# Optimization experiments

Measured on AMD Instinct MI355X. Metric: run time of the kernel, lower is better.

## Reference

```python
import jax, jax.numpy as jnp
import numpy as np

B, L, D, H = 2, 2048, 1024, 16
HD = D // H  # head_dim = 64


def _clin(xr, xi, Wr, br, Wi, bi):
    # (x_r + i x_i)(W_r + i W_i): out_r = fc_r(x_r) - fc_i(x_i); out_i = fc_r(x_i) + fc_i(x_r)
    rr = xr @ Wr.T + br
    ii = xi @ Wi.T + bi
    ri = xi @ Wr.T + br
    ir = xr @ Wi.T + bi
    return rr - ii, ri + ir


def _heads(x):
    # [B, L, D] -> [B, H, L, HD]
    return x.reshape(B, L, H, HD).transpose(0, 2, 1, 3)


def setup_inputs() -> dict:
    key = jax.random.key(0)
    ks = jax.random.split(key, 11)
    inp = {
        "x_r": jax.random.normal(ks[0], (B, L, D), jnp.float32),
        "x_i": jax.random.normal(ks[1], (B, L, D), jnp.float32),
        "attention_mask": jnp.zeros((B, 1, 1, L), jnp.float32),
    }
    names = ["Wq_r", "Wq_i", "Wk_r", "Wk_i", "Wv_r", "Wv_i", "Wo_r", "Wo_i"]
    for n, k in zip(names, ks[2:10]):
        inp[n] = jax.random.normal(k, (D, D), jnp.float32) * 0.02
        inp["b" + n[1:]] = jnp.zeros((D,), jnp.float32)
    return inp


def reference(x_r, x_i, attention_mask,
              Wq_r, bq_r, Wq_i, bq_i,
              Wk_r, bk_r, Wk_i, bk_i,
              Wv_r, bv_r, Wv_i, bv_i,
              Wo_r, bo_r, Wo_i, bo_i):
    qr, qi = _clin(x_r, x_i, Wq_r, bq_r, Wq_i, bq_i)
    kr, ki = _clin(x_r, x_i, Wk_r, bk_r, Wk_i, bk_i)
    vr, vi = _clin(x_r, x_i, Wv_r, bv_r, Wv_i, bv_i)
    q_r, q_i = _heads(qr), _heads(qi)
    k_r, k_i = _heads(kr), _heads(ki)
    v_r, v_i = _heads(vr), _heads(vi)
    # complex QK^T cross terms -> squared-magnitude interference score
    s_real = jnp.einsum('bhqd,bhkd->bhqk', q_r, k_r) + jnp.einsum('bhqd,bhkd->bhqk', q_i, k_i)
    s_imag = jnp.einsum('bhqd,bhkd->bhqk', q_i, k_r) - jnp.einsum('bhqd,bhkd->bhqk', q_r, k_i)
    interference = (s_real * s_real + s_imag * s_imag) / HD + attention_mask
    attn = jax.nn.softmax(interference, axis=-1)
    c_r = jnp.einsum('bhqk,bhkd->bhqd', attn, v_r).transpose(0, 2, 1, 3).reshape(B, L, D)
    c_i = jnp.einsum('bhqk,bhkd->bhqd', attn, v_i).transpose(0, 2, 1, 3).reshape(B, L, D)
    out_r, out_i = _clin(c_r, c_i, Wo_r, bo_r, Wo_i, bo_i)
    return out_r, out_i
```

## Files before the change

kernel.cpp:

```cpp
#include <hip/hip_runtime.h>
#include <hip/hip_bf16.h>

typedef unsigned short u16;
typedef __attribute__((ext_vector_type(8))) short bf16x8;
typedef __attribute__((ext_vector_type(8))) _Float16 f16x8;
typedef __attribute__((ext_vector_type(8))) unsigned short u16x8;
typedef __attribute__((ext_vector_type(4))) float f32x4;

__device__ __forceinline__ u16 f2b(float f) {
  _Float16 h = (_Float16)f;
  return __builtin_bit_cast(u16, h);
}

__device__ __forceinline__ f32x4 mfma16(bf16x8 a, bf16x8 b, f32x4 c) {
  return __builtin_amdgcn_mfma_f32_16x16x32_f16(
      __builtin_bit_cast(f16x8, a), __builtin_bit_cast(f16x8, b), c, 0, 0, 0);
}

#define GLD16(dst, src) __builtin_amdgcn_global_load_lds( \
    (const __attribute__((address_space(1))) void*)(src), \
    (__attribute__((address_space(3))) void*)(dst), 16, 0, 0)

__global__ void pack_x_kernel(u16* __restrict__ A1, const float* __restrict__ xr,
                              const float* __restrict__ xi) {
  const int id = blockIdx.x * 256 + threadIdx.x;
  const size_t k8 = (size_t)id * 8;
  const int n = (int)(k8 >> 11);
  const int kk = (int)(k8 & 2047);
  const float* src = (kk < 1024) ? (xr + (size_t)n * 1024 + kk)
                                 : (xi + (size_t)n * 1024 + (kk - 1024));
  float4 a = *(const float4*)src;
  float4 c = *(const float4*)(src + 4);
  u16x8 o;
  o[0] = f2b(a.x); o[1] = f2b(a.y); o[2] = f2b(a.z); o[3] = f2b(a.w);
  o[4] = f2b(c.x); o[5] = f2b(c.y); o[6] = f2b(c.z); o[7] = f2b(c.w);
  *(u16x8*)(A1 + k8) = o;
}

__global__ void pack_w_kernel(u16* __restrict__ dst, float* __restrict__ biasDst,
                              const float* __restrict__ Wr, const float* __restrict__ Wi,
                              const float* __restrict__ br, const float* __restrict__ bi,
                              int isim) {
  const int row = blockIdx.x;
  const int kk = threadIdx.x * 8;
  const int half = kk >> 10;
  const int kloc = kk & 1023;
  const float* W = (half == 0) ? (isim ? Wi : Wr) : (isim ? Wr : Wi);
  const float sgn = (half == 1 && !isim) ? -1.f : 1.f;
  const float* src = W + (size_t)row * 1024 + kloc;
  float4 a = *(const float4*)src;
  float4 c = *(const float4*)(src + 4);
  u16x8 o;
  o[0] = f2b(sgn * a.x); o[1] = f2b(sgn * a.y); o[2] = f2b(sgn * a.z); o[3] = f2b(sgn * a.w);
  o[4] = f2b(sgn * c.x); o[5] = f2b(sgn * c.y); o[6] = f2b(sgn * c.z); o[7] = f2b(sgn * c.w);
  *(u16x8*)(dst + (size_t)row * 2048 + kk) = o;
  if (threadIdx.x == 0)
    biasDst[row] = isim ? (br[row] + bi[row]) : (br[row] - bi[row]);
}

template<int OUT_F32>
__global__ __launch_bounds__(256) void gemm_bt(const u16* __restrict__ A,
                                               const u16* __restrict__ Bw,
                                               const float* __restrict__ bias,
                                               void* __restrict__ outp) {
  constexpr int K = 2048;
  __shared__ __align__(16) u16 As[128 * 64];
  __shared__ __align__(16) u16 Bs[128 * 64];
  const int tid = threadIdx.x;
  const int w = tid >> 6, l = tid & 63;
  const int l15 = l & 15, lhi = l >> 4;
  const int m0 = blockIdx.y * 128, n0 = blockIdx.x * 128;
  const int wm = w >> 1, wn = w & 1;
  f32x4 acc[4][4] = {};
  for (int kt = 0; kt < K; kt += 64) {
#pragma unroll
    for (int it = 0; it < 4; ++it) {
      const int grp = it * 4 + w;
      const int cl = grp * 64 + l;
      const int r = cl >> 3;
      const int g = (cl & 7) ^ (r & 7);
      GLD16(As + grp * 512, A + (size_t)(m0 + r) * K + kt + g * 8);
      GLD16(Bs + grp * 512, Bw + (size_t)(n0 + r) * K + kt + g * 8);
    }
    __syncthreads();
#pragma unroll
    for (int ks = 0; ks < 2; ++ks) {
      const int c = ks * 4 + lhi;
      bf16x8 af[4], bfr[4];
#pragma unroll
      for (int mf = 0; mf < 4; ++mf) {
        const int r = wm * 64 + mf * 16 + l15;
        af[mf] = *(const bf16x8*)&As[r * 64 + ((c ^ (r & 7)) << 3)];
      }
#pragma unroll
      for (int nf = 0; nf < 4; ++nf) {
        const int r = wn * 64 + nf * 16 + l15;
        bfr[nf] = *(const bf16x8*)&Bs[r * 64 + ((c ^ (r & 7)) << 3)];
      }
#pragma unroll
      for (int mf = 0; mf < 4; ++mf)
#pragma unroll
        for (int nf = 0; nf < 4; ++nf)
          acc[mf][nf] = mfma16(af[mf], bfr[nf], acc[mf][nf]);
    }
    __syncthreads();
  }
#pragma unroll
  for (int nf = 0; nf < 4; ++nf) {
    const int j = n0 + wn * 64 + nf * 16 + l15;
    const float bv = bias[j];
    const size_t obase = (size_t)(j >> 10) * (4096 * 1024) + (j & 1023);
#pragma unroll
    for (int mf = 0; mf < 4; ++mf) {
#pragma unroll
      for (int i = 0; i < 4; ++i) {
        const int row = m0 + wm * 64 + mf * 16 + lhi * 4 + i;
        const float v = acc[mf][nf][i] + bv;
        if constexpr (OUT_F32) ((float*)outp)[obase + (size_t)row * 1024] = v;
        else                   ((u16*)outp)[obase + (size_t)row * 1024] = f2b(v);
      }
    }
  }
}

__global__ void transpose_v_kernel(const u16* __restrict__ v, u16* __restrict__ vt) {
  __shared__ u16 tile[64 * 65];
  const int tt = blockIdx.x, bh = blockIdx.y, ri = blockIdx.z;
  const int b = bh >> 4, h = bh & 15;
  const size_t M1 = (size_t)4096 * 1024;
  const u16* src = v + (size_t)ri * M1;
  u16* dst = vt + (size_t)ri * 32 * 64 * 2048;
  const int t0 = tt * 64;
#pragma unroll
  for (int e = 0; e < 16; ++e) {
    const int id = e * 256 + threadIdx.x;
    const int row = id >> 6, col = id & 63;
    tile[row * 65 + col] = src[(size_t)(b * 2048 + t0 + row) * 1024 + h * 64 + col];
  }
  __syncthreads();
#pragma unroll
  for (int e = 0; e < 16; ++e) {
    const int id = e * 256 + threadIdx.x;
    const int d = id >> 6, tok = id & 63;
    dst[((size_t)bh * 64 + d) * 2048 + t0 + tok] = tile[tok * 65 + d];
  }
}

__global__ __launch_bounds__(256) void attn_kernel(const u16* __restrict__ qkv,
                                                   const u16* __restrict__ vt,
                                                   const float* __restrict__ mask,
                                                   u16* __restrict__ A2) {
  __shared__ __align__(16) u16 KVb[2][4][64 * 64];
  __shared__ __align__(16) u16 Pl[4 * 16 * 72];
  const int tid = threadIdx.x, w = tid >> 6, l = tid & 63;
  const int l15 = l & 15, lhi = l >> 4;
  const int q0 = blockIdx.x * 64;
  const int bh = blockIdx.y;
  const int b = bh >> 4, h = bh & 15;
  const size_t M1 = (size_t)4096 * 1024;
  const u16* qr_b = qkv;
  const u16* qi_b = qkv + M1;
  const u16* kr_b = qkv + 2 * M1;
  const u16* ki_b = qkv + 3 * M1;
  const u16* vtr = vt;
  const u16* vti = vt + (size_t)32 * 64 * 2048;

  const size_t qrow = (size_t)(b * 2048 + q0 + w * 16 + l15) * 1024 + h * 64;
  bf16x8 qr[2], qi[2], qrn[2];
#pragma unroll
  for (int ks = 0; ks < 2; ++ks) {
    qr[ks] = *(const bf16x8*)&qr_b[qrow + ks * 32 + lhi * 8];
    qi[ks] = *(const bf16x8*)&qi_b[qrow + ks * 32 + lhi * 8];
    qrn[ks] = qr[ks] ^ (short)0x8000;
  }
  float mrow[4], srow[4];
  f32x4 o_r[4] = {}, o_i[4] = {};
#pragma unroll
  for (int i = 0; i < 4; ++i) { mrow[i] = -1e30f; srow[i] = 0.f; }
  u16* Pw = Pl + w * (16 * 72);

  auto STAGE = [&](int tile, int bufi) {
    const int k0s = tile * 64;
#pragma unroll
    for (int it = 0; it < 2; ++it) {
      const int grp = it * 4 + w;
      const int cl = grp * 64 + l;
      const int r = cl >> 3;
      const int g = (cl & 7) ^ (r & 7);
      const size_t krow = (size_t)(b * 2048 + k0s + r) * 1024 + h * 64 + g * 8;
      const size_t vrow = (size_t)(bh * 64 + r) * 2048 + k0s + g * 8;
      GLD16(&KVb[bufi][0][grp * 512], kr_b + krow);
      GLD16(&KVb[bufi][1][grp * 512], ki_b + krow);
      GLD16(&KVb[bufi][2][grp * 512], vtr + vrow);
      GLD16(&KVb[bufi][3][grp * 512], vti + vrow);
    }
  };

  STAGE(0, 0);
  for (int kt = 0; kt < 32; ++kt) {
    const int cur = kt & 1;
    const int k0 = kt * 64;
    __syncthreads();
    if (kt < 31) STAGE(kt + 1, cur ^ 1);
    const u16* Kr = &KVb[cur][0][0];
    const u16* Ki = &KVb[cur][1][0];
    const u16* Vr = &KVb[cur][2][0];
    const u16* Vi = &KVb[cur][3][0];
    f32x4 sr[4] = {}, si[4] = {};
    __builtin_amdgcn_s_setprio(1);
#pragma unroll
    for (int nf = 0; nf < 4; ++nf) {
      const int krr = nf * 16 + l15;
      const int sw = krr & 7;
#pragma unroll
      for (int ks = 0; ks < 2; ++ks) {
        const int c = ks * 4 + lhi;
        const int off = krr * 64 + ((c ^ sw) << 3);
        bf16x8 kfr = *(const bf16x8*)&Kr[off];
        bf16x8 kfi = *(const bf16x8*)&Ki[off];
        sr[nf] = mfma16(qr[ks], kfr, sr[nf]);
        sr[nf] = mfma16(qi[ks], kfi, sr[nf]);
        si[nf] = mfma16(qi[ks], kfr, si[nf]);
        si[nf] = mfma16(qrn[ks], kfi, si[nf]);
      }
    }
    __builtin_amdgcn_s_setprio(0);
    float t[4][4];
#pragma unroll
    for (int nf = 0; nf < 4; ++nf) {
      const float mk = mask[b * 2048 + k0 + nf * 16 + l15];
#pragma unroll
      for (int i = 0; i < 4; ++i)
        t[nf][i] = (sr[nf][i] * sr[nf][i] + si[nf][i] * si[nf][i]) * 0.015625f + mk;
    }
    float pmax[4];
#pragma unroll
    for (int i = 0; i < 4; ++i) {
      float v = fmaxf(fmaxf(t[0][i], t[1][i]), fmaxf(t[2][i], t[3][i]));
      v = fmaxf(v, __shfl_xor(v, 1, 64));
      v = fmaxf(v, __shfl_xor(v, 2, 64));
      v = fmaxf(v, __shfl_xor(v, 4, 64));
      v = fmaxf(v, __shfl_xor(v, 8, 64));
      pmax[i] = v;
    }
    bool grow = false;
#pragma unroll
    for (int i = 0; i < 4; ++i) grow |= (pmax[i] > mrow[i] + 8.f);
    if (__any(grow)) {
#pragma unroll
      for (int i = 0; i < 4; ++i) {
        const float mn = fmaxf(mrow[i], pmax[i]);
        const float sc = __expf(mrow[i] - mn);
        mrow[i] = mn;
        srow[i] *= sc;
#pragma unroll
        for (int nf = 0; nf < 4; ++nf) { o_r[nf][i] *= sc; o_i[nf][i] *= sc; }
      }
    }
    float p[4][4];
#pragma unroll
    for (int nf = 0; nf < 4; ++nf)
#pragma unroll
      for (int i = 0; i < 4; ++i) {
        p[nf][i] = __expf(t[nf][i] - mrow[i]);
        srow[i] += p[nf][i];
      }
#pragma unroll
    for (int nf = 0; nf < 4; ++nf)
#pragma unroll
      for (int i = 0; i < 4; ++i)
        Pw[(lhi * 4 + i) * 72 + nf * 16 + l15] = f2b(p[nf][i]);
    __builtin_amdgcn_s_setprio(1);
#pragma unroll
    for (int ks = 0; ks < 2; ++ks) {
      bf16x8 pa = *(const bf16x8*)&Pw[l15 * 72 + ks * 32 + lhi * 8];
      const int c = ks * 4 + lhi;
#pragma unroll
      for (int nf = 0; nf < 4; ++nf) {
        const int vr = nf * 16 + l15;
        const int off = vr * 64 + ((c ^ (vr & 7)) << 3);
        bf16x8 vfr = *(const bf16x8*)&Vr[off];
        bf16x8 vfi = *(const bf16x8*)&Vi[off];
        o_r[nf] = mfma16(pa, vfr, o_r[nf]);
        o_i[nf] = mfma16(pa, vfi, o_i[nf]);
      }
    }
    __builtin_amdgcn_s_setprio(0);
  }
  float inv[4];
#pragma unroll
  for (int i = 0; i < 4; ++i) {
    float v = srow[i];
    v += __shfl_xor(v, 1, 64);
    v += __shfl_xor(v, 2, 64);
    v += __shfl_xor(v, 4, 64);
    v += __shfl_xor(v, 8, 64);
    inv[i] = 1.f / v;
  }
  const int rowbase = b * 2048 + q0 + w * 16 + lhi * 4;
#pragma unroll
  for (int nf = 0; nf < 4; ++nf) {
    const int col = h * 64 + nf * 16 + l15;
#pragma unroll
    for (int i = 0; i < 4; ++i) {
      const size_t rw = (size_t)(rowbase + i) * 2048;
      A2[rw + col] = f2b(o_r[nf][i] * inv[i]);
      A2[rw + 1024 + col] = f2b(o_i[nf][i] * inv[i]);
    }
  }
}

extern "C" void kernel_launch(void* const* d_in, const int* in_sizes, int n_in,
                              void* d_out, int out_size, void* d_ws, size_t ws_size,
                              hipStream_t stream) {
  (void)in_sizes; (void)n_in; (void)out_size; (void)ws_size;
  const float* x_r  = (const float*)d_in[0];
  const float* x_i  = (const float*)d_in[1];
  const float* mask = (const float*)d_in[2];
  const float* Wq_r = (const float*)d_in[3];
  const float* bq_r = (const float*)d_in[4];
  const float* Wq_i = (const float*)d_in[5];
  const float* bq_i = (const float*)d_in[6];
  const float* Wk_r = (const float*)d_in[7];
  const float* bk_r = (const float*)d_in[8];
  const float* Wk_i = (const float*)d_in[9];
  const float* bk_i = (const float*)d_in[10];
  const float* Wv_r = (const float*)d_in[11];
  const float* bv_r = (const float*)d_in[12];
  const float* Wv_i = (const float*)d_in[13];
  const float* bv_i = (const float*)d_in[14];
  const float* Wo_r = (const float*)d_in[15];
  const float* bo_r = (const float*)d_in[16];
  const float* Wo_i = (const float*)d_in[17];
  const float* bo_i = (const float*)d_in[18];

  char* ws = (char*)d_ws;
  const size_t M1 = (size_t)4096 * 1024;
  u16* A    = (u16*)(ws);
  u16* B1   = (u16*)(ws + (16u << 20));
  u16* vt   = (u16*)(ws + (16u << 20));
  u16* B2   = (u16*)(ws + (32u << 20));
  u16* qkv  = (u16*)(ws + (40u << 20));
  float* bias1 = (float*)(ws + (88u << 20));
  float* bias2 = (float*)(ws + (88u << 20) + (1u << 15));

  pack_x_kernel<<<4096, 256, 0, stream>>>(A, x_r, x_i);
  pack_w_kernel<<<1024, 256, 0, stream>>>(B1 + 0 * (size_t)1024 * 2048, bias1 + 0,    Wq_r, Wq_i, bq_r, bq_i, 0);
  pack_w_kernel<<<1024, 256, 0, stream>>>(B1 + 1 * (size_t)1024 * 2048, bias1 + 1024, Wq_r, Wq_i, bq_r, bq_i, 1);
  pack_w_kernel<<<1024, 256, 0, stream>>>(B1 + 2 * (size_t)1024 * 2048, bias1 + 2048, Wk_r, Wk_i, bk_r, bk_i, 0);
  pack_w_kernel<<<1024, 256, 0, stream>>>(B1 + 3 * (size_t)1024 * 2048, bias1 + 3072, Wk_r, Wk_i, bk_r, bk_i, 1);
  pack_w_kernel<<<1024, 256, 0, stream>>>(B1 + 4 * (size_t)1024 * 2048, bias1 + 4096, Wv_r, Wv_i, bv_r, bv_i, 0);
  pack_w_kernel<<<1024, 256, 0, stream>>>(B1 + 5 * (size_t)1024 * 2048, bias1 + 5120, Wv_r, Wv_i, bv_r, bv_i, 1);

  gemm_bt<0><<<dim3(48, 32), 256, 0, stream>>>(A, B1, bias1, qkv);

  transpose_v_kernel<<<dim3(32, 32, 2), 256, 0, stream>>>(qkv + 4 * M1, vt);
  pack_w_kernel<<<1024, 256, 0, stream>>>(B2,                      bias2,        Wo_r, Wo_i, bo_r, bo_i, 0);
  pack_w_kernel<<<1024, 256, 0, stream>>>(B2 + (size_t)1024 * 2048, bias2 + 1024, Wo_r, Wo_i, bo_r, bo_i, 1);

  attn_kernel<<<dim3(32, 32), 256, 0, stream>>>(qkv, vt, mask, A);

  gemm_bt<1><<<dim3(16, 32), 256, 0, stream>>>(A, B2, bias2, d_out);
}
```

Measured before the change: 478.2 us.

## Fuse V transpose into QKV GEMM epilogue, batch weight packing, shrink attention tiles

The QKV GEMM epilogue now writes V directly in transposed layout, which removes the separate transpose kernel. Weight packing is batched into two grid launches instead of eight. The attention kernel drops to 32-key tiles with a per-wave staging split, a smaller LDS footprint and launch bounds targeting 4 blocks per CU. Softmax now runs in base 2 via v_exp_f32 with the log2e scale folded into the score constant, and the rescale threshold is raised to match. Smaller tiles mean twice as many iterations and barriers, which may offset the occupancy gain.

After: 486.5 us. Within noise of the previous version (+1.7%).

```diff
diff --git a/kernel.cpp b/kernel.cpp
--- a/kernel.cpp
+++ b/kernel.cpp
@@ -15,6 +15,10 @@
 __device__ __forceinline__ f32x4 mfma16(bf16x8 a, bf16x8 b, f32x4 c) {
   return __builtin_amdgcn_mfma_f32_16x16x32_f16(
       __builtin_bit_cast(f16x8, a), __builtin_bit_cast(f16x8, b), c, 0, 0, 0);
+}
+
+__device__ __forceinline__ float fexp2(float x) {
+  float r; asm("v_exp_f32 %0, %1" : "=v"(r) : "v"(x)); return r;
 }
 
 #define GLD16(dst, src) __builtin_amdgcn_global_load_lds( \
@@ -37,32 +41,44 @@
   *(u16x8*)(A1 + k8) = o;
 }
 
-__global__ void pack_w_kernel(u16* __restrict__ dst, float* __restrict__ biasDst,
-                              const float* __restrict__ Wr, const float* __restrict__ Wi,
-                              const float* __restrict__ br, const float* __restrict__ bi,
-                              int isim) {
+struct PWArgs {
+  const float* Wr[4]; const float* Wi[4];
+  const float* br[4]; const float* bi[4];
+};
+
+__global__ void pack_w_all(PWArgs a, int sbase, u16* __restrict__ B1,
+                           u16* __restrict__ B2, float* __restrict__ bias1,
+                           float* __restrict__ bias2) {
+  const int s = sbase + blockIdx.y;
+  const int wi = s >> 1, isim = s & 1;
+  u16* dst = (s < 6) ? (B1 + (size_t)s * (1024 * 2048))
+                     : (B2 + (size_t)(s - 6) * (1024 * 2048));
+  float* biasDst = (s < 6) ? (bias1 + s * 1024) : (bias2 + (s - 6) * 1024);
   const int row = blockIdx.x;
   const int kk = threadIdx.x * 8;
   const int half = kk >> 10;
   const int kloc = kk & 1023;
-  const float* W = (half == 0) ? (isim ? Wi : Wr) : (isim ? Wr : Wi);
+  const float* W = (half == 0) ? (isim ? a.Wi[wi] : a.Wr[wi])
+                               : (isim ? a.Wr[wi] : a.Wi[wi]);
   const float sgn = (half == 1 && !isim) ? -1.f : 1.f;
   const float* src = W + (size_t)row * 1024 + kloc;
-  float4 a = *(const float4*)src;
+  float4 x = *(const float4*)src;
   float4 c = *(const float4*)(src + 4);
   u16x8 o;
-  o[0] = f2b(sgn * a.x); o[1] = f2b(sgn * a.y); o[2] = f2b(sgn * a.z); o[3] = f2b(sgn * a.w);
+  o[0] = f2b(sgn * x.x); o[1] = f2b(sgn * x.y); o[2] = f2b(sgn * x.z); o[3] = f2b(sgn * x.w);
   o[4] = f2b(sgn * c.x); o[5] = f2b(sgn * c.y); o[6] = f2b(sgn * c.z); o[7] = f2b(sgn * c.w);
   *(u16x8*)(dst + (size_t)row * 2048 + kk) = o;
   if (threadIdx.x == 0)
-    biasDst[row] = isim ? (br[row] + bi[row]) : (br[row] - bi[row]);
-}
-
-template<int OUT_F32>
+    biasDst[row] = isim ? (a.br[wi][row] + a.bi[wi][row])
+                        : (a.br[wi][row] - a.bi[wi][row]);
+}
+
+template<int MODE>
 __global__ __launch_bounds__(256) void gemm_bt(const u16* __restrict__ A,
                                                const u16* __restrict__ Bw,
                                                const float* __restrict__ bias,
-                                               void* __restrict__ outp) {
+                                               void* __restrict__ outp,
+                                               u16* __restrict__ vtp) {
   constexpr int K = 2048;
   __shared__ __align__(16) u16 As[128 * 64];
   __shared__ __align__(16) u16 Bs[128 * 64];
@@ -109,49 +125,49 @@
   for (int nf = 0; nf < 4; ++nf) {
     const int j = n0 + wn * 64 + nf * 16 + l15;
     const float bv = bias[j];
-    const size_t obase = (size_t)(j >> 10) * (4096 * 1024) + (j & 1023);
-#pragma unroll
-    for (int mf = 0; mf < 4; ++mf) {
-#pragma unroll
-      for (int i = 0; i < 4; ++i) {
-        const int row = m0 + wm * 64 + mf * 16 + lhi * 4 + i;
-        const float v = acc[mf][nf][i] + bv;
-        if constexpr (OUT_F32) ((float*)outp)[obase + (size_t)row * 1024] = v;
-        else                   ((u16*)outp)[obase + (size_t)row * 1024] = f2b(v);
-      }
-    }
-  }
-}
-
-__global__ void transpose_v_kernel(const u16* __restrict__ v, u16* __restrict__ vt) {
-  __shared__ u16 tile[64 * 65];
-  const int tt = blockIdx.x, bh = blockIdx.y, ri = blockIdx.z;
-  const int b = bh >> 4, h = bh & 15;
-  const size_t M1 = (size_t)4096 * 1024;
-  const u16* src = v + (size_t)ri * M1;
-  u16* dst = vt + (size_t)ri * 32 * 64 * 2048;
-  const int t0 = tt * 64;
-#pragma unroll
-  for (int e = 0; e < 16; ++e) {
-    const int id = e * 256 + threadIdx.x;
-    const int row = id >> 6, col = id & 63;
-    tile[row * 65 + col] = src[(size_t)(b * 2048 + t0 + row) * 1024 + h * 64 + col];
-  }
-  __syncthreads();
-#pragma unroll
-  for (int e = 0; e < 16; ++e) {
-    const int id = e * 256 + threadIdx.x;
-    const int d = id >> 6, tok = id & 63;
-    dst[((size_t)bh * 64 + d) * 2048 + t0 + tok] = tile[tok * 65 + d];
-  }
-}
-
-__global__ __launch_bounds__(256) void attn_kernel(const u16* __restrict__ qkv,
-                                                   const u16* __restrict__ vt,
-                                                   const float* __restrict__ mask,
-                                                   u16* __restrict__ A2) {
-  __shared__ __align__(16) u16 KVb[2][4][64 * 64];
-  __shared__ __align__(16) u16 Pl[4 * 16 * 72];
+    if constexpr (MODE == 1) {
+      const size_t obase = (size_t)(j >> 10) * (4096 * 1024) + (j & 1023);
+#pragma unroll
+      for (int mf = 0; mf < 4; ++mf)
+#pragma unroll
+        for (int i = 0; i < 4; ++i) {
+          const int row = m0 + wm * 64 + mf * 16 + lhi * 4 + i;
+          ((float*)outp)[obase + (size_t)row * 1024] = acc[mf][nf][i] + bv;
+        }
+    } else {
+      if (j < 4096) {
+        const size_t obase = (size_t)(j >> 10) * (4096 * 1024) + (j & 1023);
+#pragma unroll
+        for (int mf = 0; mf < 4; ++mf)
+#pragma unroll
+          for (int i = 0; i < 4; ++i) {
+            const int row = m0 + wm * 64 + mf * 16 + lhi * 4 + i;
+            ((u16*)outp)[obase + (size_t)row * 1024] = f2b(acc[mf][nf][i] + bv);
+          }
+      } else {
+        const int jv = j - 4096;
+        const size_t vb = (size_t)(jv >> 10) * 4194304 +
+                          (size_t)((jv >> 6) & 15) * 131072 +
+                          (size_t)(jv & 63) * 2048;
+#pragma unroll
+        for (int mf = 0; mf < 4; ++mf)
+#pragma unroll
+          for (int i = 0; i < 4; ++i) {
+            const int row = m0 + wm * 64 + mf * 16 + lhi * 4 + i;
+            const int b2 = row >> 11, tok = row & 2047;
+            vtp[vb + (size_t)b2 * 2097152 + tok] = f2b(acc[mf][nf][i] + bv);
+          }
+      }
+    }
+  }
+}
+
+__global__ __launch_bounds__(256, 4) void attn_kernel(const u16* __restrict__ qkv,
+                                                      const u16* __restrict__ vt,
+                                                      const float* __restrict__ mask,
+                                                      u16* __restrict__ A2) {
+  __shared__ __align__(16) u16 KVb[2][4][2048];
+  __shared__ __align__(16) u16 Pl[4][16 * 40];
   const int tid = threadIdx.x, w = tid >> 6, l = tid & 63;
   const int l15 = l & 15, lhi = l >> 4;
   const int q0 = blockIdx.x * 64;
@@ -164,6 +180,8 @@
   const u16* ki_b = qkv + 3 * M1;
   const u16* vtr = vt;
   const u16* vti = vt + (size_t)32 * 64 * 2048;
+  constexpr float LOG2E = 1.4426950408889634f;
+  constexpr float C2 = 0.015625f * LOG2E;
 
   const size_t qrow = (size_t)(b * 2048 + q0 + w * 16 + l15) * 1024 + h * 64;
   bf16x8 qr[2], qi[2], qrn[2];
@@ -177,45 +195,54 @@
   f32x4 o_r[4] = {}, o_i[4] = {};
 #pragma unroll
   for (int i = 0; i < 4; ++i) { mrow[i] = -1e30f; srow[i] = 0.f; }
-  u16* Pw = Pl + w * (16 * 72);
+  u16* Pw = Pl[w];
 
   auto STAGE = [&](int tile, int bufi) {
-    const int k0s = tile * 64;
-#pragma unroll
-    for (int it = 0; it < 2; ++it) {
-      const int grp = it * 4 + w;
-      const int cl = grp * 64 + l;
-      const int r = cl >> 3;
-      const int g = (cl & 7) ^ (r & 7);
-      const size_t krow = (size_t)(b * 2048 + k0s + r) * 1024 + h * 64 + g * 8;
-      const size_t vrow = (size_t)(bh * 64 + r) * 2048 + k0s + g * 8;
-      GLD16(&KVb[bufi][0][grp * 512], kr_b + krow);
-      GLD16(&KVb[bufi][1][grp * 512], ki_b + krow);
-      GLD16(&KVb[bufi][2][grp * 512], vtr + vrow);
-      GLD16(&KVb[bufi][3][grp * 512], vti + vrow);
+    const int k0s = tile * 32;
+    if (w < 2) {
+      const u16* src = w ? ki_b : kr_b;
+      u16* dstb = &KVb[bufi][w][0];
+#pragma unroll
+      for (int it = 0; it < 4; ++it) {
+        const int cl = it * 64 + l;
+        const int r = cl >> 3;
+        const int g = (cl & 7) ^ (r & 7);
+        GLD16(dstb + it * 512, src + (size_t)(b * 2048 + k0s + r) * 1024 + h * 64 + g * 8);
+      }
+    } else {
+      const u16* src = (w == 3) ? vti : vtr;
+      u16* dstb = &KVb[bufi][w][0];
+#pragma unroll
+      for (int it = 0; it < 4; ++it) {
+        const int cl = it * 64 + l;
+        const int r = cl >> 2;
+        const int g = (cl & 3) ^ ((r >> 1) & 3);
+        GLD16(dstb + it * 512, src + (size_t)(bh * 64 + r) * 2048 + k0s + g * 8);
+      }
     }
   };
 
   STAGE(0, 0);
-  for (int kt = 0; kt < 32; ++kt) {
+#pragma unroll 2
+  for (int kt = 0; kt < 64; ++kt) {
     const int cur = kt & 1;
-    const int k0 = kt * 64;
+    const int k0 = kt * 32;
     __syncthreads();
-    if (kt < 31) STAGE(kt + 1, cur ^ 1);
+    if (kt < 63) STAGE(kt + 1, cur ^ 1);
     const u16* Kr = &KVb[cur][0][0];
     const u16* Ki = &KVb[cur][1][0];
     const u16* Vr = &KVb[cur][2][0];
     const u16* Vi = &KVb[cur][3][0];
-    f32x4 sr[4] = {}, si[4] = {};
+    f32x4 sr[2] = {}, si[2] = {};
     __builtin_amdgcn_s_setprio(1);
 #pragma unroll
-    for (int nf = 0; nf < 4; ++nf) {
-      const int krr = nf * 16 + l15;
-      const int sw = krr & 7;
+    for (int nf = 0; nf < 2; ++nf) {
+      const int rk = nf * 16 + l15;
+      const int sw = rk & 7;
 #pragma unroll
       for (int ks = 0; ks < 2; ++ks) {
         const int c = ks * 4 + lhi;
-        const int off = krr * 64 + ((c ^ sw) << 3);
+        const int off = rk * 64 + ((c ^ sw) << 3);
         bf16x8 kfr = *(const bf16x8*)&Kr[off];
         bf16x8 kfi = *(const bf16x8*)&Ki[off];
         sr[nf] = mfma16(qr[ks], kfr, sr[nf]);
@@ -225,18 +252,20 @@
       }
     }
     __builtin_amdgcn_s_setprio(0);
-    float t[4][4];
-#pragma unroll
-    for (int nf = 0; nf < 4; ++nf) {
-      const float mk = mask[b * 2048 + k0 + nf * 16 + l15];
-#pragma unroll
-      for (int i = 0; i < 4; ++i)
-        t[nf][i] = (sr[nf][i] * sr[nf][i] + si[nf][i] * si[nf][i]) * 0.015625f + mk;
+    float t[2][4];
+#pragma unroll
+    for (int nf = 0; nf < 2; ++nf) {
+      const float mkl = mask[b * 2048 + k0 + nf * 16 + l15] * LOG2E;
+#pragma unroll
+      for (int i = 0; i < 4; ++i) {
+        const float ss = fmaf(si[nf][i], si[nf][i], sr[nf][i] * sr[nf][i]);
+        t[nf][i] = fmaf(ss, C2, mkl);
+      }
     }
     float pmax[4];
 #pragma unroll
     for (int i = 0; i < 4; ++i) {
-      float v = fmaxf(fmaxf(t[0][i], t[1][i]), fmaxf(t[2][i], t[3][i]));
+      float v = fmaxf(t[0][i], t[1][i]);
       v = fmaxf(v, __shfl_xor(v, 1, 64));
       v = fmaxf(v, __shfl_xor(v, 2, 64));
       v = fmaxf(v, __shfl_xor(v, 4, 64));
@@ -245,45 +274,41 @@
     }
     bool grow = false;
 #pragma unroll
-    for (int i = 0; i < 4; ++i) grow |= (pmax[i] > mrow[i] + 8.f);
+    for (int i = 0; i < 4; ++i) grow |= (pmax[i] > mrow[i] + 11.f);
     if (__any(grow)) {
 #pragma unroll
       for (int i = 0; i < 4; ++i) {
         const float mn = fmaxf(mrow[i], pmax[i]);
-        const float sc = __expf(mrow[i] - mn);
+        const float sc = fexp2(mrow[i] - mn);
         mrow[i] = mn;
         srow[i] *= sc;
 #pragma unroll
         for (int nf = 0; nf < 4; ++nf) { o_r[nf][i] *= sc; o_i[nf][i] *= sc; }
       }
     }
-    float p[4][4];
-#pragma unroll
-    for (int nf = 0; nf < 4; ++nf)
+    float p[2][4];
+#pragma unroll
+    for (int nf = 0; nf < 2; ++nf)
 #pragma unroll
       for (int i = 0; i < 4; ++i) {
-        p[nf][i] = __expf(t[nf][i] - mrow[i]);
+        p[nf][i] = fexp2(t[nf][i] - mrow[i]);
         srow[i] += p[nf][i];
       }
 #pragma unroll
-    for (int nf = 0; nf < 4; ++nf)
+    for (int nf = 0; nf < 2; ++nf)
 #pragma unroll
       for (int i = 0; i < 4; ++i)
-        Pw[(lhi * 4 + i) * 72 + nf * 16 + l15] = f2b(p[nf][i]);
+        Pw[(lhi * 4 + i) * 40 + nf * 16 + l15] = f2b(p[nf][i]);
+    bf16x8 pa = *(const bf16x8*)&Pw[l15 * 40 + lhi * 8];
     __builtin_amdgcn_s_setprio(1);
 #pragma unroll
-    for (int ks = 0; ks < 2; ++ks) {
-      bf16x8 pa = *(const bf16x8*)&Pw[l15 * 72 + ks * 32 + lhi * 8];
-      const int c = ks * 4 + lhi;
-#pragma unroll
-      for (int nf = 0; nf < 4; ++nf) {
-        const int vr = nf * 16 + l15;
-        const int off = vr * 64 + ((c ^ (vr & 7)) << 3);
-        bf16x8 vfr = *(const bf16x8*)&Vr[off];
-        bf16x8 vfi = *(const bf16x8*)&Vi[off];
-        o_r[nf] = mfma16(pa, vfr, o_r[nf]);
-        o_i[nf] = mfma16(pa, vfi, o_i[nf]);
-      }
+    for (int nf = 0; nf < 4; ++nf) {
+      const int d = nf * 16 + l15;
+      const int off = d * 32 + ((lhi ^ ((d >> 1) & 3)) << 3);
+      bf16x8 vfr = *(const bf16x8*)&Vr[off];
+      bf16x8 vfi = *(const bf16x8*)&Vi[off];
+      o_r[nf] = mfma16(pa, vfr, o_r[nf]);
+      o_i[nf] = mfma16(pa, vfi, o_i[nf]);
     }
     __builtin_amdgcn_s_setprio(0);
   }
@@ -317,48 +342,34 @@
   const float* x_r  = (const float*)d_in[0];
   const float* x_i  = (const float*)d_in[1];
   const float* mask = (const float*)d_in[2];
-  const float* Wq_r = (const float*)d_in[3];
-  const float* bq_r = (const float*)d_in[4];
-  const float* Wq_i = (const float*)d_in[5];
-  const float* bq_i = (const float*)d_in[6];
-  const float* Wk_r = (const float*)d_in[7];
-  const float* bk_r = (const float*)d_in[8];
-  const float* Wk_i = (const float*)d_in[9];
-  const float* bk_i = (const float*)d_in[10];
-  const float* Wv_r = (const float*)d_in[11];
-  const float* bv_r = (const float*)d_in[12];
-  const float* Wv_i = (const float*)d_in[13];
-  const float* bv_i = (const float*)d_in[14];
-  const float* Wo_r = (const float*)d_in[15];
-  const float* bo_r = (const float*)d_in[16];
-  const float* Wo_i = (const float*)d_in[17];
-  const float* bo_i = (const float*)d_in[18];
+
+  PWArgs pw;
+  pw.Wr[0] = (const float*)d_in[3];  pw.br[0] = (const float*)d_in[4];
+  pw.Wi[0] = (const float*)d_in[5];  pw.bi[0] = (const float*)d_in[6];
+  pw.Wr[1] = (const float*)d_in[7];  pw.br[1] = (const float*)d_in[8];
+  pw.Wi[1] = (const float*)d_in[9];  pw.bi[1] = (const float*)d_in[10];
+  pw.Wr[2] = (const float*)d_in[11]; pw.br[2] = (const float*)d_in[12];
+  pw.Wi[2] = (const float*)d_in[13]; pw.bi[2] = (const float*)d_in[14];
+  pw.Wr[3] = (const float*)d_in[15]; pw.br[3] = (const float*)d_in[16];
+  pw.Wi[3] = (const float*)d_in[17]; pw.bi[3] = (const float*)d_in[18];
 
   char* ws = (char*)d_ws;
-  const size_t M1 = (size_t)4096 * 1024;
-  u16* A    = (u16*)(ws);
-  u16* B1   = (u16*)(ws + (16u << 20));
-  u16* vt   = (u16*)(ws + (16u << 20));
-  u16* B2   = (u16*)(ws + (32u << 20));
-  u16* qkv  = (u16*)(ws + (40u << 20));
+  u16* A     = (u16*)(ws);
+  u16* B1    = (u16*)(ws + (16u << 20));
+  u16* B2    = (u16*)(ws + (16u << 20));
+  u16* qkvp  = (u16*)(ws + (40u << 20));
+  u16* vtp   = (u16*)(ws + (72u << 20));
   float* bias1 = (float*)(ws + (88u << 20));
   float* bias2 = (float*)(ws + (88u << 20) + (1u << 15));
 
   pack_x_kernel<<<4096, 256, 0, stream>>>(A, x_r, x_i);
-  pack_w_kernel<<<1024, 256, 0, stream>>>(B1 + 0 * (size_t)1024 * 2048, bias1 + 0,    Wq_r, Wq_i, bq_r, bq_i, 0);
-  pack_w_kernel<<<1024, 256, 0, stream>>>(B1 + 1 * (size_t)1024 * 2048, bias1 + 1024, Wq_r, Wq_i, bq_r, bq_i, 1);
-  pack_w_kernel<<<1024, 256, 0, stream>>>(B1 + 2 * (size_t)1024 * 2048, bias1 + 2048, Wk_r, Wk_i, bk_r, bk_i, 0);
-  pack_w_kernel<<<1024, 256, 0, stream>>>(B1 + 3 * (size_t)1024 * 2048, bias1 + 3072, Wk_r, Wk_i, bk_r, bk_i, 1);
-  pack_w_kernel<<<1024, 256, 0, stream>>>(B1 + 4 * (size_t)1024 * 2048, bias1 + 4096, Wv_r, Wv_i, bv_r, bv_i, 0);
-  pack_w_kernel<<<1024, 256, 0, stream>>>(B1 + 5 * (size_t)1024 * 2048, bias1 + 5120, Wv_r, Wv_i, bv_r, bv_i, 1);
-
-  gemm_bt<0><<<dim3(48, 32), 256, 0, stream>>>(A, B1, bias1, qkv);
-
-  transpose_v_kernel<<<dim3(32, 32, 2), 256, 0, stream>>>(qkv + 4 * M1, vt);
-  pack_w_kernel<<<1024, 256, 0, stream>>>(B2,                      bias2,        Wo_r, Wo_i, bo_r, bo_i, 0);
-  pack_w_kernel<<<1024, 256, 0, stream>>>(B2 + (size_t)1024 * 2048, bias2 + 1024, Wo_r, Wo_i, bo_r, bo_i, 1);
-
-  attn_kernel<<<dim3(32, 32), 256, 0, stream>>>(qkv, vt, mask, A);
-
-  gemm_bt<1><<<dim3(16, 32), 256, 0, stream>>>(A, B2, bias2, d_out);
-}
+  pack_w_all<<<dim3(1024, 6), 256, 0, stream>>>(pw, 0, B1, B2, bias1, bias2);
+
+  gemm_bt<0><<<dim3(48, 32), 256, 0, stream>>>(A, B1, bias1, qkvp, vtp);
+
+  pack_w_all<<<dim3(1024, 2), 256, 0, stream>>>(pw, 6, B1, B2, bias1, bias2);
+
+  attn_kernel<<<dim3(32, 32), 256, 0, stream>>>(qkvp, vtp, mask, A);
+
+  gemm_bt<1><<<dim3(16, 32), 256, 0, stream>>>(A, B2, bias2, d_out, nullptr);
+}
```
